# Performance work log

Hardware: AMD Instinct MI355X
Metric: run time of the kernel (lower is better)

Reference implementation:

```python
import jax, jax.numpy as jnp
import numpy as np

N_NODES = 100000
N_EDGES = 1600000
F_IN = 128
HID = 128
N_CLASSES = 32
N_GRAPHS = 1024


def setup_inputs() -> dict:
    key = jax.random.key(0)
    ks = jax.random.split(key, 8)
    x = jax.random.normal(ks[0], (N_NODES, F_IN), dtype=jnp.float32)
    edge_index = jax.random.randint(ks[1], (2, N_EDGES), 0, N_NODES, dtype=jnp.int64)
    batch = jnp.sort(jax.random.randint(ks[2], (N_NODES,), 0, N_GRAPHS, dtype=jnp.int64))
    W1 = jax.random.normal(ks[3], (F_IN, HID), dtype=jnp.float32) * (1.0 / np.sqrt(F_IN))
    b1 = jnp.zeros((HID,), dtype=jnp.float32)
    W2 = jax.random.normal(ks[4], (HID, HID), dtype=jnp.float32) * (1.0 / np.sqrt(HID))
    b2 = jnp.zeros((HID,), dtype=jnp.float32)
    Wf = jax.random.normal(ks[5], (HID, N_CLASSES), dtype=jnp.float32) * (1.0 / np.sqrt(HID))
    bf = jnp.zeros((N_CLASSES,), dtype=jnp.float32)
    return {"x": x, "edge_index": edge_index, "batch": batch,
            "W1": W1, "b1": b1, "W2": W2, "b2": b2, "Wf": Wf, "bf": bf}


def _gcn_conv(x, W, b, src, dst, n_nodes):
    # GCNConv: linear transform, add self-loops, symmetric normalization,
    # scatter-add aggregation, then bias.
    h = x @ W                                   # [N, H]
    loop = jnp.arange(n_nodes, dtype=src.dtype)
    s = jnp.concatenate([src, loop])            # [E+N]
    d = jnp.concatenate([dst, loop])
    deg = jax.ops.segment_sum(jnp.ones_like(d, dtype=h.dtype), d, num_segments=n_nodes)
    dinv = jnp.where(deg > 0, jax.lax.rsqrt(deg), jnp.zeros_like(deg))
    norm = dinv[s] * dinv[d]                    # [E+N]
    msgs = h[s] * norm[:, None]                 # gather + scale
    out = jax.ops.segment_sum(msgs, d, num_segments=n_nodes)  # scatter-add
    return out + b


def reference(x, edge_index, batch, W1, b1, W2, b2, Wf, bf):
    src, dst = edge_index[0], edge_index[1]
    n = x.shape[0]
    h = _gcn_conv(x, W1, b1, src, dst, n)
    h = jax.nn.relu(h)
    # F.dropout(training=False) -> identity (inference baseline)
    h = _gcn_conv(h, W2, b2, src, dst, n)
    # global_mean_pool over graph ids
    pooled_sum = jax.ops.segment_sum(h, batch, num_segments=N_GRAPHS)       # [G, H]
    counts = jax.ops.segment_sum(jnp.ones((n,), h.dtype), batch, num_segments=N_GRAPHS)
    pooled = pooled_sum / jnp.clip(counts, 1.0)[:, None]
    return pooled @ Wf + bf                      # [G, C]
```

## Files before the change

kernel.cpp:

```cpp
#include <hip/hip_runtime.h>
#include <hip/hip_bf16.h>

#define N_NODES   100000
#define N_EDGES   1600000
#define FDIM      128
#define N_GRAPHS  1024
#define N_CLASSES 32
#define SCAN_BLK  1024
#define M_PAD     100032

typedef __attribute__((ext_vector_type(8))) short short8v;
typedef __attribute__((ext_vector_type(4))) float f32x4;

__device__ __forceinline__ float bflo(unsigned u){ union{unsigned i; float f;} c; c.i = u << 16; return c.f; }
__device__ __forceinline__ float bfhi(unsigned u){ union{unsigned i; float f;} c; c.i = u & 0xffff0000u; return c.f; }
__device__ __forceinline__ unsigned short f2bf(float f){
    union{float f; unsigned u;} c{f};
    return (unsigned short)((c.u + 0x7fffu + ((c.u >> 16) & 1u)) >> 16);
}
__device__ __forceinline__ unsigned packbf2(float a, float b){
    return (unsigned)f2bf(a) | ((unsigned)f2bf(b) << 16);
}

__global__ void k_f2bf(const float* __restrict__ in, unsigned* __restrict__ out, int n2) {
    int i = blockIdx.x * blockDim.x + threadIdx.x;
    if (i < n2) {
        float2 v = ((const float2*)in)[i];
        out[i] = packbf2(v.x, v.y);
    }
}

__global__ void k_wt(const float* __restrict__ W, unsigned short* __restrict__ Wt) {
    int i = blockIdx.x * blockDim.x + threadIdx.x;
    int k = i >> 7, n = i & 127;
    Wt[n * 128 + k] = f2bf(W[i]);
}

__global__ void k_count(const int* __restrict__ dst, int* __restrict__ indeg, int E) {
    int i = blockIdx.x * blockDim.x + threadIdx.x;
    if (i < E) atomicAdd(&indeg[dst[i]], 1);
}

__global__ void k_dinv(const int* __restrict__ indeg, float* __restrict__ dinv, int n) {
    int i = blockIdx.x * blockDim.x + threadIdx.x;
    if (i < n) dinv[i] = rsqrtf((float)(indeg[i] + 1));
}

__global__ void k_scan1(const int* __restrict__ in, int* __restrict__ out,
                        int* __restrict__ bsums, int n) {
    __shared__ int lds[256];
    int blk = blockIdx.x, t = threadIdx.x;
    int base = blk * SCAN_BLK + t * 4;
    int v[4];
#pragma unroll
    for (int i = 0; i < 4; ++i) v[i] = (base + i < n) ? in[base + i] : 0;
    int local = v[0] + v[1] + v[2] + v[3];
    lds[t] = local;
    __syncthreads();
    for (int off = 1; off < 256; off <<= 1) {
        int x = lds[t];
        int y = (t >= off) ? lds[t - off] : 0;
        __syncthreads();
        lds[t] = x + y;
        __syncthreads();
    }
    int excl = lds[t] - local;
    if (t == 255) bsums[blk] = lds[255];
    int run = excl;
#pragma unroll
    for (int i = 0; i < 4; ++i) {
        if (base + i < n) { out[base + i] = run; run += v[i]; }
    }
}

__global__ void k_scan2(int* __restrict__ bsums, int nb) {
    __shared__ int lds[256];
    int t = threadIdx.x;
    int orig = (t < nb) ? bsums[t] : 0;
    lds[t] = orig;
    __syncthreads();
    for (int off = 1; off < 256; off <<= 1) {
        int x = lds[t];
        int y = (t >= off) ? lds[t - off] : 0;
        __syncthreads();
        lds[t] = x + y;
        __syncthreads();
    }
    if (t < nb) bsums[t] = lds[t] - orig;
}

__global__ void k_scan3(int* __restrict__ rp, const int* __restrict__ boffs, int n, int E) {
    int i = blockIdx.x * blockDim.x + threadIdx.x;
    if (i < n) rp[i] += boffs[i / SCAN_BLK];
    if (i == n) rp[n] = E;
}

__global__ void k_fill(const int* __restrict__ src, const int* __restrict__ dst,
                       const int* __restrict__ rp, int* __restrict__ cursor,
                       int* __restrict__ col, float* __restrict__ wgt,
                       const float* __restrict__ dinv, int E) {
    int i = blockIdx.x * blockDim.x + threadIdx.x;
    if (i < E) {
        int d = dst[i], s = src[i];
        int p = atomicAdd(&cursor[d], 1);
        int idx = rp[d] + p;
        col[idx] = s;
        wgt[idx] = dinv[d] * dinv[s];
    }
}

#define AGG_BODY(X2, V)                                                          \
    int lane = threadIdx.x & 63;                                                 \
    int V = (blockIdx.x << 2) + (threadIdx.x >> 6);                              \
    if (V >= N_NODES) return;                                                    \
    float dv = dinv[V];                                                          \
    unsigned xs = X2[V * 64 + lane];                                             \
    float wself = dv * dv;                                                       \
    float a0x = wself * bflo(xs), a0y = wself * bfhi(xs);                        \
    float a1x = 0.f, a1y = 0.f, a2x = 0.f, a2y = 0.f, a3x = 0.f, a3y = 0.f;     \
    int e = rp[V], e1 = rp[V + 1];                                               \
    if (e + 4 <= e1) {                                                           \
        int s0 = col[e], s1 = col[e+1], s2 = col[e+2], s3 = col[e+3];            \
        float w0 = wgt[e], w1 = wgt[e+1], w2 = wgt[e+2], w3 = wgt[e+3];          \
        while (true) {                                                           \
            int en = e + 4;                                                      \
            bool more = (en + 4 <= e1);                                          \
            int t0, t1, t2, t3; float y0, y1, y2, y3;                            \
            if (more) {                                                          \
                t0 = col[en]; t1 = col[en+1]; t2 = col[en+2]; t3 = col[en+3];    \
                y0 = wgt[en]; y1 = wgt[en+1]; y2 = wgt[en+2]; y3 = wgt[en+3];    \
            }                                                                    \
            unsigned u0 = X2[s0*64 + lane], u1 = X2[s1*64 + lane];               \
            unsigned u2 = X2[s2*64 + lane], u3 = X2[s3*64 + lane];               \
            a0x += w0 * bflo(u0); a0y += w0 * bfhi(u0);                          \
            a1x += w1 * bflo(u1); a1y += w1 * bfhi(u1);                          \
            a2x += w2 * bflo(u2); a2y += w2 * bfhi(u2);                          \
            a3x += w3 * bflo(u3); a3y += w3 * bfhi(u3);                          \
            e = en;                                                              \
            if (!more) break;                                                    \
            s0 = t0; s1 = t1; s2 = t2; s3 = t3;                                  \
            w0 = y0; w1 = y1; w2 = y2; w3 = y3;                                  \
        }                                                                        \
    }                                                                            \
    for (; e < e1; ++e) {                                                        \
        int s = col[e]; float w = wgt[e];                                        \
        unsigned u = X2[s*64 + lane];                                            \
        a0x += w * bflo(u); a0y += w * bfhi(u);                                  \
    }                                                                            \
    float ax = (a0x + a1x) + (a2x + a3x);                                        \
    float ay = (a0y + a1y) + (a2y + a3y);

__global__ __launch_bounds__(256) void k_agg1(
    const unsigned* __restrict__ X2, unsigned* __restrict__ O2,
    const int* __restrict__ rp, const int* __restrict__ col,
    const float* __restrict__ wgt, const float* __restrict__ dinv)
{
    AGG_BODY(X2, v)
    O2[v * 64 + lane] = packbf2(ax, ay);
}

__global__ __launch_bounds__(256) void k_agg2(
    const unsigned* __restrict__ X2,
    const int* __restrict__ rp, const int* __restrict__ col,
    const float* __restrict__ wgt, const float* __restrict__ dinv,
    const int* __restrict__ batch, float* __restrict__ P, int* __restrict__ cnt)
{
    AGG_BODY(X2, v)
    int g = batch[v];
    atomicAdd(&P[(size_t)g * FDIM + 2 * lane],     ax);
    atomicAdd(&P[(size_t)g * FDIM + 2 * lane + 1], ay);
    if (lane == 0) atomicAdd(&cnt[g], 1);
}

__global__ __launch_bounds__(256) void k_gemm_mfma(
    const unsigned short* __restrict__ A, const unsigned short* __restrict__ Wt,
    const float* __restrict__ bias, unsigned short* __restrict__ B)
{
    int lane = threadIdx.x & 63;
    int wv = threadIdx.x >> 6;
    size_t row0 = (size_t)blockIdx.x * 64 + (size_t)wv * 16;
    int r = lane & 15, g = lane >> 4;

    short8v af[4];
    const unsigned short* arow = A + (row0 + r) * FDIM + g * 8;
#pragma unroll
    for (int ks = 0; ks < 4; ++ks)
        af[ks] = *(const short8v*)(arow + ks * 32);

    f32x4 acc[8];
#pragma unroll
    for (int ct = 0; ct < 8; ++ct) {
        f32x4 a = {0.f, 0.f, 0.f, 0.f};
        const unsigned short* wrow = Wt + (ct * 16 + r) * FDIM + g * 8;
#pragma unroll
        for (int ks = 0; ks < 4; ++ks) {
            short8v bfr = *(const short8v*)(wrow + ks * 32);
            a = __builtin_amdgcn_mfma_f32_16x16x32_bf16(af[ks], bfr, a, 0, 0, 0);
        }
        acc[ct] = a;
    }

#pragma unroll
    for (int ct = 0; ct < 8; ++ct) {
        int c = ct * 16 + r;
        float bs = bias[c];
#pragma unroll
        for (int i = 0; i < 4; ++i) {
            size_t row = row0 + g * 4 + i;
            if (row < N_NODES) {
                float vv = fmaxf(acc[ct][i] + bs, 0.f);
                B[row * FDIM + c] = f2bf(vv);
            }
        }
    }
}

__global__ void k_wcomb(const float* __restrict__ W2, const float* __restrict__ Wf,
                        const float* __restrict__ b2, const float* __restrict__ bf,
                        float* __restrict__ Wc, float* __restrict__ bc) {
    int idx = blockIdx.x * blockDim.x + threadIdx.x;
    if (idx < 128 * 32) {
        int k = idx >> 5, c = idx & 31;
        float acc = 0.0f;
        for (int m = 0; m < 128; ++m) acc += W2[k * 128 + m] * Wf[m * 32 + c];
        Wc[idx] = acc;
    }
    if (idx < 32) {
        float acc = bf[idx];
        for (int m = 0; m < 128; ++m) acc += b2[m] * Wf[m * 32 + idx];
        bc[idx] = acc;
    }
}

__global__ void k_final(const float* __restrict__ P, const int* __restrict__ cnt,
                        const float* __restrict__ Wc, const float* __restrict__ bc,
                        const float* __restrict__ bf, float* __restrict__ out) {
    __shared__ float p[128];
    int g = blockIdx.x, t = threadIdx.x;
    int c_ = cnt[g];
    float inv = (c_ > 0) ? 1.0f / (float)c_ : 0.0f;
    p[t] = P[(size_t)g * FDIM + t] * inv;
    __syncthreads();
    if (t < N_CLASSES) {
        float acc = (c_ > 0) ? bc[t] : bf[t];
#pragma unroll
        for (int k = 0; k < 128; ++k) acc = fmaf(p[k], Wc[k * 32 + t], acc);
        out[(size_t)g * N_CLASSES + t] = acc;
    }
}

extern "C" void kernel_launch(void* const* d_in, const int* in_sizes, int n_in,
                              void* d_out, int out_size, void* d_ws, size_t ws_size,
                              hipStream_t stream) {
    const float* x    = (const float*)d_in[0];
    const int*   ei   = (const int*)d_in[1];
    const int*   batch= (const int*)d_in[2];
    const float* W1   = (const float*)d_in[3];
    const float* b1   = (const float*)d_in[4];
    const float* W2   = (const float*)d_in[5];
    const float* b2   = (const float*)d_in[6];
    const float* Wf   = (const float*)d_in[7];
    const float* bf   = (const float*)d_in[8];
    const int* src = ei;
    const int* dst = ei + N_EDGES;

    char* w = (char*)d_ws;
    auto alloc = [&](size_t bytes) { char* p = w; w += (bytes + 255) & ~255ull; return p; };
    int*      indeg  = (int*)     alloc((size_t)N_NODES * 4);
    float*    dinv   = (float*)   alloc((size_t)N_NODES * 4);
    int*      rp     = (int*)     alloc((size_t)(N_NODES + 1) * 4);
    int*      cursor = (int*)     alloc((size_t)N_NODES * 4);
    int*      bsums  = (int*)     alloc(1024 * 4);
    int*      col    = (int*)     alloc((size_t)N_EDGES * 4);
    float*    wgt    = (float*)   alloc((size_t)N_EDGES * 4);
    unsigned* xh     = (unsigned*)alloc((size_t)N_NODES * 64 * 4);
    unsigned* Ab     = (unsigned*)alloc((size_t)M_PAD  * 64 * 4);
    unsigned* Bb     = (unsigned*)alloc((size_t)N_NODES * 64 * 4);
    unsigned short* Wt = (unsigned short*)alloc(128 * 128 * 2);
    float*    P      = (float*)   alloc((size_t)N_GRAPHS * FDIM * 4);
    int*      cnt    = (int*)     alloc((size_t)N_GRAPHS * 4);
    float*    Wc     = (float*)   alloc(128 * 32 * 4);
    float*    bc     = (float*)   alloc(32 * 4);

    hipMemsetAsync(indeg,  0, (size_t)N_NODES * 4, stream);
    hipMemsetAsync(cursor, 0, (size_t)N_NODES * 4, stream);
    hipMemsetAsync(P,      0, (size_t)N_GRAPHS * FDIM * 4, stream);
    hipMemsetAsync(cnt,    0, (size_t)N_GRAPHS * 4, stream);

    const int nbScan = (N_NODES + SCAN_BLK - 1) / SCAN_BLK;

    k_f2bf<<<(N_NODES * 64 + 255) / 256, 256, 0, stream>>>(x, xh, N_NODES * 64);
    k_wt  <<<64, 256, 0, stream>>>(W1, Wt);

    k_count<<<(N_EDGES + 255) / 256, 256, 0, stream>>>(dst, indeg, N_EDGES);
    k_dinv <<<(N_NODES + 255) / 256, 256, 0, stream>>>(indeg, dinv, N_NODES);
    k_scan1<<<nbScan, 256, 0, stream>>>(indeg, rp, bsums, N_NODES);
    k_scan2<<<1, 256, 0, stream>>>(bsums, nbScan);
    k_scan3<<<(N_NODES + 1 + 255) / 256, 256, 0, stream>>>(rp, bsums, N_NODES, N_EDGES);
    k_fill <<<(N_EDGES + 255) / 256, 256, 0, stream>>>(src, dst, rp, cursor, col, wgt, dinv, N_EDGES);

    k_agg1<<<(N_NODES + 3) / 4, 256, 0, stream>>>(xh, Ab, rp, col, wgt, dinv);
    k_gemm_mfma<<<M_PAD / 64, 256, 0, stream>>>((const unsigned short*)Ab, Wt, b1,
                                                (unsigned short*)Bb);

    k_wcomb<<<16, 256, 0, stream>>>(W2, Wf, b2, bf, Wc, bc);

    k_agg2<<<(N_NODES + 3) / 4, 256, 0, stream>>>(Bb, rp, col, wgt, dinv, batch, P, cnt);

    k_final<<<N_GRAPHS, 128, 0, stream>>>(P, cnt, Wc, bc, bf, (float*)d_out);
}
```

Before: 523.3 us.

## Split each node's edge list across four 16-lane groups with 16-byte gathers

The aggregation kernels now split each wavefront into four 16-lane groups. Each group handles a strided subset of the node's edges (self-loop included) and loads a full 256-byte bf16 row with uint4 loads per lane instead of 4-byte loads. Partial sums are combined with cross-lane shuffles, and the pooled atomics are spread across groups. This aims to raise memory-level parallelism and load width in the gather, at the cost of extra shuffle reductions and some idle lanes for low-degree nodes.

```diff
diff --git a/kernel.cpp b/kernel.cpp
--- a/kernel.cpp
+++ b/kernel.cpp
@@ -20,6 +20,13 @@
 }
 __device__ __forceinline__ unsigned packbf2(float a, float b){
     return (unsigned)f2bf(a) | ((unsigned)f2bf(b) << 16);
+}
+
+__device__ __forceinline__ void fma8(float* acc, float w, uint4 u) {
+    acc[0] += w * bflo(u.x); acc[1] += w * bfhi(u.x);
+    acc[2] += w * bflo(u.y); acc[3] += w * bfhi(u.y);
+    acc[4] += w * bflo(u.z); acc[5] += w * bfhi(u.z);
+    acc[6] += w * bflo(u.w); acc[7] += w * bfhi(u.w);
 }
 
 __global__ void k_f2bf(const float* __restrict__ in, unsigned* __restrict__ out, int n2) {
@@ -109,54 +116,55 @@
     }
 }
 
-#define AGG_BODY(X2, V)                                                          \
+#define AGG3_BODY(X2)                                                            \
     int lane = threadIdx.x & 63;                                                 \
-    int V = (blockIdx.x << 2) + (threadIdx.x >> 6);                              \
-    if (V >= N_NODES) return;                                                    \
-    float dv = dinv[V];                                                          \
-    unsigned xs = X2[V * 64 + lane];                                             \
-    float wself = dv * dv;                                                       \
-    float a0x = wself * bflo(xs), a0y = wself * bfhi(xs);                        \
-    float a1x = 0.f, a1y = 0.f, a2x = 0.f, a2y = 0.f, a3x = 0.f, a3y = 0.f;     \
-    int e = rp[V], e1 = rp[V + 1];                                               \
-    if (e + 4 <= e1) {                                                           \
-        int s0 = col[e], s1 = col[e+1], s2 = col[e+2], s3 = col[e+3];            \
-        float w0 = wgt[e], w1 = wgt[e+1], w2 = wgt[e+2], w3 = wgt[e+3];          \
-        while (true) {                                                           \
-            int en = e + 4;                                                      \
-            bool more = (en + 4 <= e1);                                          \
-            int t0, t1, t2, t3; float y0, y1, y2, y3;                            \
-            if (more) {                                                          \
-                t0 = col[en]; t1 = col[en+1]; t2 = col[en+2]; t3 = col[en+3];    \
-                y0 = wgt[en]; y1 = wgt[en+1]; y2 = wgt[en+2]; y3 = wgt[en+3];    \
-            }                                                                    \
-            unsigned u0 = X2[s0*64 + lane], u1 = X2[s1*64 + lane];               \
-            unsigned u2 = X2[s2*64 + lane], u3 = X2[s3*64 + lane];               \
-            a0x += w0 * bflo(u0); a0y += w0 * bfhi(u0);                          \
-            a1x += w1 * bflo(u1); a1y += w1 * bfhi(u1);                          \
-            a2x += w2 * bflo(u2); a2y += w2 * bfhi(u2);                          \
-            a3x += w3 * bflo(u3); a3y += w3 * bfhi(u3);                          \
-            e = en;                                                              \
-            if (!more) break;                                                    \
-            s0 = t0; s1 = t1; s2 = t2; s3 = t3;                                  \
-            w0 = y0; w1 = y1; w2 = y2; w3 = y3;                                  \
-        }                                                                        \
+    int grp  = lane >> 4;                                                        \
+    int fl   = lane & 15;                                                        \
+    int v = (blockIdx.x << 2) + (threadIdx.x >> 6);                              \
+    if (v >= N_NODES) return;                                                    \
+    float dv = dinv[v];                                                          \
+    int e0 = rp[v];                                                              \
+    int L  = rp[v + 1] - e0 + 1;                               \
+    float acc[8] = {0.f,0.f,0.f,0.f,0.f,0.f,0.f,0.f};                            \
+    int i = grp;                                                                 \
+    int sA = -1, sB = -1; float wA = 0.f, wB = 0.f;                              \
+    if (i < L) {                                                                 \
+        if (i == 0) { sA = v; wA = dv * dv; }                                    \
+        else        { sA = col[e0 + i - 1]; wA = wgt[e0 + i - 1]; }              \
     }                                                                            \
-    for (; e < e1; ++e) {                                                        \
-        int s = col[e]; float w = wgt[e];                                        \
-        unsigned u = X2[s*64 + lane];                                            \
-        a0x += w * bflo(u); a0y += w * bfhi(u);                                  \
+    if (i + 4 < L) { sB = col[e0 + i + 3]; wB = wgt[e0 + i + 3]; }               \
+    while (sA >= 0) {                                                            \
+        int sC = -1, sD = -1; float wC = 0.f, wD = 0.f;                          \
+        if (i + 8  < L) { sC = col[e0 + i + 7];  wC = wgt[e0 + i + 7]; }         \
+        if (i + 12 < L) { sD = col[e0 + i + 11]; wD = wgt[e0 + i + 11]; }        \
+        uint4 uA = *(const uint4*)(X2 + (size_t)sA * 64 + fl * 4);               \
+        uint4 uB;                                                                \
+        bool hB = (sB >= 0);                                                     \
+        if (hB) uB = *(const uint4*)(X2 + (size_t)sB * 64 + fl * 4);             \
+        fma8(acc, wA, uA);                                                       \
+        if (hB) fma8(acc, wB, uB);                                               \
+        i += 8; sA = sC; wA = wC; sB = sD; wB = wD;                              \
     }                                                                            \
-    float ax = (a0x + a1x) + (a2x + a3x);                                        \
-    float ay = (a0y + a1y) + (a2y + a3y);
+    _Pragma("unroll")                                                            \
+    for (int j = 0; j < 8; ++j) {                                                \
+        acc[j] += __shfl_xor(acc[j], 16, 64);                                    \
+        acc[j] += __shfl_xor(acc[j], 32, 64);                                    \
+    }
 
 __global__ __launch_bounds__(256) void k_agg1(
     const unsigned* __restrict__ X2, unsigned* __restrict__ O2,
     const int* __restrict__ rp, const int* __restrict__ col,
     const float* __restrict__ wgt, const float* __restrict__ dinv)
 {
-    AGG_BODY(X2, v)
-    O2[v * 64 + lane] = packbf2(ax, ay);
+    AGG3_BODY(X2)
+    if (grp == 0) {
+        uint4 o;
+        o.x = packbf2(acc[0], acc[1]);
+        o.y = packbf2(acc[2], acc[3]);
+        o.z = packbf2(acc[4], acc[5]);
+        o.w = packbf2(acc[6], acc[7]);
+        *(uint4*)(O2 + (size_t)v * 64 + fl * 4) = o;
+    }
 }
 
 __global__ __launch_bounds__(256) void k_agg2(
@@ -165,10 +173,10 @@
     const float* __restrict__ wgt, const float* __restrict__ dinv,
     const int* __restrict__ batch, float* __restrict__ P, int* __restrict__ cnt)
 {
-    AGG_BODY(X2, v)
+    AGG3_BODY(X2)
     int g = batch[v];
-    atomicAdd(&P[(size_t)g * FDIM + 2 * lane],     ax);
-    atomicAdd(&P[(size_t)g * FDIM + 2 * lane + 1], ay);
+    atomicAdd(&P[(size_t)g * FDIM + fl * 8 + 2 * grp],     acc[2 * grp]);
+    atomicAdd(&P[(size_t)g * FDIM + fl * 8 + 2 * grp + 1], acc[2 * grp + 1]);
     if (lane == 0) atomicAdd(&cnt[g], 1);
 }
 
```

Result: faster. 492.5 us (-5.9%).
